# Kernel optimization log

Measured on AMD Instinct MI355X. Metric: run time of the kernel, lower is better.

The kernel has to match this reference:

```python
import jax, jax.numpy as jnp
import numpy as np

N_NODES = 10000
N_EDGES = 160000
K = 3  # Chebyshev filter order
DIMS = [(782, 16), (16, 32), (32, 64), (64, 128), (128, 19)]


def _cheb_norm(edge_index, num_nodes):
    # PyG ChebConv norm with normalization='sym', lambda_max=2.0:
    # scaled Laplacian L_hat = 2L/lambda_max - I = -D^{-1/2} A D^{-1/2} (off-diag), diag = 0
    src, dst = edge_index[0], edge_index[1]
    w = jnp.ones(src.shape, dtype=jnp.float32)
    deg = jax.ops.segment_sum(w, src, num_segments=num_nodes)
    dinv = jnp.where(deg > 0, 1.0 / jnp.sqrt(deg), 0.0)  # masked_fill(inf) -> 0
    return -dinv[src] * dinv[dst]


def _spmm(norm, src, dst, x, num_nodes):
    # out[i] = sum_{e: dst[e]==i} norm[e] * x[src[e]]
    return jax.ops.segment_sum(norm[:, None] * x[src], dst, num_segments=num_nodes)


def _cheb_conv(x, src, dst, norm, W, b):
    # W: [K, Fin, Fout]; Chebyshev recursion T0=x, T1=L_hat x, Tk=2 L_hat T_{k-1} - T_{k-2}
    n = x.shape[0]
    Tx0 = x
    out = Tx0 @ W[0]
    Tx1 = _spmm(norm, src, dst, Tx0, n)
    out = out + Tx1 @ W[1]
    for k in range(2, W.shape[0]):
        Tx2 = 2.0 * _spmm(norm, src, dst, Tx1, n) - Tx0
        out = out + Tx2 @ W[k]
        Tx0, Tx1 = Tx1, Tx2
    return out + b


def setup_inputs() -> dict:
    key = jax.random.key(0)
    ks = jax.random.split(key, 2 + len(DIMS))
    x = jax.random.normal(ks[0], (N_NODES, 782), dtype=jnp.float32)
    edge_index = jax.random.randint(ks[1], (2, N_EDGES), 0, N_NODES)
    inp = {"x": x, "edge_index": edge_index}
    for i, (fi, fo) in enumerate(DIMS):
        inp[f"W{i+1}"] = jax.random.normal(ks[2 + i], (K, fi, fo), dtype=jnp.float32) / np.float32(np.sqrt(fi * K))
        inp[f"b{i+1}"] = jnp.zeros((fo,), dtype=jnp.float32)
    return inp


def reference(x, edge_index, W1, b1, W2, b2, W3, b3, W4, b4, W5, b5):
    src, dst = edge_index[0], edge_index[1]
    norm = _cheb_norm(edge_index, x.shape[0])
    h = jax.nn.relu(_cheb_conv(x, src, dst, norm, W1, b1))
    h = jax.nn.relu(_cheb_conv(h, src, dst, norm, W2, b2))
    h = jax.nn.relu(_cheb_conv(h, src, dst, norm, W3, b3))
    h = jax.nn.relu(_cheb_conv(h, src, dst, norm, W4, b4))
    h = _cheb_conv(h, src, dst, norm, W5, b5)
    return jax.nn.softmax(h, axis=-1)
```

## Files before the change

kernel.cpp:

```cpp
#include <hip/hip_runtime.h>
#include <math.h>

#define NN 10000
#define NE 160000
#define CAP 128
#define NT 256
#define WC1_TOTAL (782 * 48)
#define WC5_TOTAL (128 * 60)
#define L1_SPLITS 12
#define L1_KCHUNK 66
#define CNT_BLKS 625

struct MegaParams {
  const float* x;
  const int* src;
  const int* dst;
  const float* W1; const float* b1;
  const float* W2; const float* b2;
  const float* W3; const float* b3;
  const float* W4; const float* b4;
  const float* W5; const float* b5;
  int* deg; int* cnt; int* bsrc;
  float* dinv; float* wc1; float* wc5;
  float* ABC1; float* E1; float* B2; float* B3; float* B4;
  float* H4; float* ABC5; float* E5; float* P;
  float* out;
};

__device__ __forceinline__ void wcat_one(const float* __restrict__ W,
                                         float* __restrict__ Wc,
                                         int i, int Fin, int F, int Fp) {
  int w3 = 3 * Fp;
  int row = i / w3;
  int c = i - row * w3;
  int sec = c / Fp;
  int f = c - sec * Fp;
  float v = 0.0f;
  if (f < F) {
    if (sec == 0)      v = W[row * F + f] - W[2 * Fin * F + row * F + f];
    else if (sec == 1) v = W[Fin * F + row * F + f];
    else               v = W[2 * Fin * F + row * F + f];
  }
  Wc[i] = v;
}

struct Row8 { float4 lo, hi; };

template <bool AL16>
__device__ __forceinline__ Row8 ld_row8(const float* __restrict__ X, int ldx,
                                        int gr, int M, int kc, int kend) {
  Row8 r;
  r.lo = make_float4(0.f, 0.f, 0.f, 0.f);
  r.hi = make_float4(0.f, 0.f, 0.f, 0.f);
  if (gr < M && kc < kend) {
    const float* xp = X + (size_t)gr * ldx + kc;
    if (kc + 8 <= kend) {
      if (AL16) {
        r.lo = ((const float4*)xp)[0];
        r.hi = ((const float4*)xp)[1];
      } else {
        float2 a = *(const float2*)xp;
        float2 b = *(const float2*)(xp + 2);
        float2 c = *(const float2*)(xp + 4);
        float2 d = *(const float2*)(xp + 6);
        r.lo = make_float4(a.x, a.y, b.x, b.y);
        r.hi = make_float4(c.x, c.y, d.x, d.y);
      }
    } else {
      int rem = kend - kc;
      r.lo.x = xp[0];
      if (rem > 1) r.lo.y = xp[1];
      if (rem > 2) r.lo.z = xp[2];
      if (rem > 3) r.lo.w = xp[3];
      if (rem > 4) r.hi.x = xp[4];
      if (rem > 5) r.hi.y = xp[5];
      if (rem > 6) r.hi.z = xp[6];
    }
  }
  return r;
}

__device__ __forceinline__ float comp8(const Row8& r, int k) {
  switch (k) {
    case 0: return r.lo.x; case 1: return r.lo.y;
    case 2: return r.lo.z; case 3: return r.lo.w;
    case 4: return r.hi.x; case 5: return r.hi.y;
    case 6: return r.hi.z; default: return r.hi.w;
  }
}

__device__ __forceinline__ float rlane(float v, int i) {
  return __int_as_float(__builtin_amdgcn_readlane(__float_as_int(v), i));
}

template <int TN, bool AL16, bool DIRECT>
__device__ void gemm_stage(const float* __restrict__ X, int ldx,
                           const float* __restrict__ W, int ldw,
                           float* __restrict__ Y, int ldy,
                           const float* __restrict__ bias, int relu,
                           int M, int Kd, int Nd, int kchunk, int nk,
                           int tile0, int tstride, float* Ws) {
  int ntR = (M + NT - 1) / NT;
  int ntC = Nd / TN;
  int ntRC = ntR * ntC;
  int ntiles = ntRC * nk;
  constexpr int W4 = TN / 4;
  for (int tile = tile0; tile < ntiles; tile += tstride) {
    int tz = tile / ntRC;
    int rm = tile - tz * ntRC;
    int tc = rm / ntR;
    int tr = rm - tc * ntR;
    int row0 = tr * NT;
    int col0 = tc * TN;
    int k0 = tz * kchunk;
    int kend = k0 + kchunk;
    if (kend > Kd) kend = Kd;
    int k8 = ((kend - k0) + 7) & ~7;
    __syncthreads();
    for (int idx = threadIdx.x; idx < k8 * W4; idx += NT) {
      int wk = idx / W4;
      int wc = (idx - wk * W4) * 4;
      float4 wv = make_float4(0.f, 0.f, 0.f, 0.f);
      if (k0 + wk < kend)
        wv = *(const float4*)(W + (size_t)(k0 + wk) * ldw + col0 + wc);
      *(float4*)(Ws + wk * TN + wc) = wv;
    }
    __syncthreads();
    float acc[TN];
#pragma unroll
    for (int c = 0; c < TN; c++) acc[c] = 0.f;
    int r = row0 + threadIdx.x;
    int nch = k8 >> 3;
    Row8 cur = ld_row8<AL16>(X, ldx, r, M, k0, kend);
    for (int ci = 0; ci < nch; ci++) {
      Row8 nxt = cur;
      if (ci + 1 < nch) nxt = ld_row8<AL16>(X, ldx, r, M, k0 + (ci + 1) * 8, kend);
      int kb = ci << 3;
#pragma unroll
      for (int k = 0; k < 8; k++) {
        float x0 = comp8(cur, k);
        const float* wr = Ws + (kb + k) * TN;
#pragma unroll
        for (int c = 0; c < TN; c += 4) {
          float4 wv = *(const float4*)(wr + c);
          acc[c + 0] += x0 * wv.x; acc[c + 1] += x0 * wv.y;
          acc[c + 2] += x0 * wv.z; acc[c + 3] += x0 * wv.w;
        }
      }
      cur = nxt;
    }
    if (r < M) {
      if (DIRECT) {
        float* yr = Y + (size_t)r * ldy + col0;
#pragma unroll
        for (int c = 0; c < TN; c += 4) {
          float4 v;
          v.x = acc[c + 0] + (bias ? bias[col0 + c + 0] : 0.f);
          v.y = acc[c + 1] + (bias ? bias[col0 + c + 1] : 0.f);
          v.z = acc[c + 2] + (bias ? bias[col0 + c + 2] : 0.f);
          v.w = acc[c + 3] + (bias ? bias[col0 + c + 3] : 0.f);
          if (relu) {
            v.x = fmaxf(v.x, 0.f); v.y = fmaxf(v.y, 0.f);
            v.z = fmaxf(v.z, 0.f); v.w = fmaxf(v.w, 0.f);
          }
          *(float4*)(yr + c) = v;
        }
      } else {
        float* pr = Y + ((size_t)tz * M + r) * Nd + col0;
#pragma unroll
        for (int c = 0; c < TN; c += 4)
          *(float4*)(pr + c) = make_float4(acc[c], acc[c + 1], acc[c + 2], acc[c + 3]);
      }
    }
  }
}

__device__ void spmm_stage(const int* __restrict__ cnt,
                           const int* __restrict__ bsrc,
                           const float* __restrict__ dinv,
                           const float* __restrict__ X, int ldx,
                           float* __restrict__ Y, int ldy,
                           const float* __restrict__ add, int lda,
                           const float* __restrict__ bias,
                           float alpha, float beta,
                           int C_log2, int Fstore, int relu, int do_softmax) {
  int wv = threadIdx.x >> 6;
  int lane = threadIdx.x & 63;
  int C = 1 << C_log2;
  int chunk = lane & (C - 1);
  int eslot = lane >> C_log2;
  int Epar = 64 >> C_log2;
  for (int node = blockIdx.x * 4 + wv; node < NN; node += gridDim.x * 4) {
    int cn = cnt[node]; if (cn > CAP) cn = CAP;
    float dn = dinv[node];
    int j0 = node << 7;
    int j1 = j0 + cn;
    float sx = 0.f, sy = 0.f, sz = 0.f, sw = 0.f;
    for (int j = j0 + eslot; j < j1; j += Epar) {
      int sn = bsrc[j];
      float w = dinv[sn];
      float4 xv = *(const float4*)(X + (size_t)sn * ldx + (chunk << 2));
      sx += w * xv.x; sy += w * xv.y; sz += w * xv.z; sw += w * xv.w;
    }
    for (int st = C; st < 64; st <<= 1) {
      sx += __shfl_xor(sx, st);
      sy += __shfl_xor(sy, st);
      sz += __shfl_xor(sz, st);
      sw += __shfl_xor(sw, st);
    }
    if (eslot == 0) {
      float am = -alpha * dn;
      int f0 = chunk << 2;
      float4 u = make_float4(am * sx, am * sy, am * sz, am * sw);
      if (add) {
        float4 av = *(const float4*)(add + (size_t)node * lda + f0);
        u.x += beta * av.x; u.y += beta * av.y; u.z += beta * av.z; u.w += beta * av.w;
      }
      if (bias) {
        if (f0 + 0 < Fstore) u.x += bias[f0 + 0];
        if (f0 + 1 < Fstore) u.y += bias[f0 + 1];
        if (f0 + 2 < Fstore) u.z += bias[f0 + 2];
        if (f0 + 3 < Fstore) u.w += bias[f0 + 3];
      }
      if (!do_softmax) {
        if (relu) {
          u.x = fmaxf(u.x, 0.f); u.y = fmaxf(u.y, 0.f);
          u.z = fmaxf(u.z, 0.f); u.w = fmaxf(u.w, 0.f);
        }
        if (f0 + 4 <= Fstore) {
          *(float4*)(Y + (size_t)node * ldy + f0) = u;
        } else {
          float vv[4] = {u.x, u.y, u.z, u.w};
#pragma unroll
          for (int c = 0; c < 4; c++)
            if (f0 + c < Fstore) Y[(size_t)node * ldy + f0 + c] = vv[c];
        }
      } else {
        float v[4] = {u.x, u.y, u.z, u.w};
        float mx = -INFINITY;
#pragma unroll
        for (int c = 0; c < 4; c++)
          if (f0 + c < Fstore) mx = fmaxf(mx, v[c]);
        mx = fmaxf(mx, __shfl_xor(mx, 1));
        mx = fmaxf(mx, __shfl_xor(mx, 2));
        mx = fmaxf(mx, __shfl_xor(mx, 4));
        float e[4];
        float s = 0.f;
#pragma unroll
        for (int c = 0; c < 4; c++) {
          e[c] = (f0 + c < Fstore) ? __expf(v[c] - mx) : 0.f;
          s += e[c];
        }
        s += __shfl_xor(s, 1);
        s += __shfl_xor(s, 2);
        s += __shfl_xor(s, 4);
        float inv = 1.f / s;
#pragma unroll
        for (int c = 0; c < 4; c++) {
          int f = f0 + c;
          if (f < Fstore) Y[(size_t)node * ldy + f] = e[c] * inv;
        }
      }
    }
  }
}

template <int F, int C_log2, int LD, int KK, int FOUT, int LDO>
__global__ __launch_bounds__(NT) void k_fused_t2gemm(
    const int* __restrict__ cnt, const int* __restrict__ bsrc,
    const float* __restrict__ dinv, const float* __restrict__ B,
    const float* __restrict__ W, const float* __restrict__ bias,
    float* __restrict__ Y) {
  int wv = threadIdx.x >> 6;
  int lane = threadIdx.x & 63;
  constexpr int C = 1 << C_log2;
  int chunk = lane & (C - 1);
  int eslot = lane >> C_log2;
  constexpr int Epar = 64 >> C_log2;
  int col = lane % FOUT;
  float wr[KK];
#pragma unroll
  for (int k = 0; k < KK; k++) wr[k] = W[k * FOUT + col];
  float bb = bias[col];
  for (int node = blockIdx.x * 4 + wv; node < NN; node += gridDim.x * 4) {
    int cn = cnt[node]; if (cn > CAP) cn = CAP;
    float dn = dinv[node];
    int j0 = node << 7, j1 = j0 + cn;
    float sx = 0.f, sy = 0.f, sz = 0.f, sw = 0.f;
    for (int j = j0 + eslot; j < j1; j += Epar) {
      int sn = bsrc[j];
      float w = dinv[sn];
      float4 xv = *(const float4*)(B + (size_t)sn * LD + F + (chunk << 2));
      sx += w * xv.x; sy += w * xv.y; sz += w * xv.z; sw += w * xv.w;
    }
#pragma unroll
    for (int st = C; st < 64; st <<= 1) {
      sx += __shfl_xor(sx, st);
      sy += __shfl_xor(sy, st);
      sz += __shfl_xor(sz, st);
      sw += __shfl_xor(sw, st);
    }
    int ridx = (lane < 2 * F) ? lane : (lane - 2 * F);
    float rv0 = B[(size_t)node * LD + ridx];
    int f = (KK == 48) ? (lane - 2 * F) : lane;
    int cc = (f >> 2) & (C - 1);
    float a0 = __shfl(sx, cc), a1 = __shfl(sy, cc);
    float a2 = __shfl(sz, cc), a3 = __shfl(sw, cc);
    int comp = f & 3;
    float Ssel = (comp == 0) ? a0 : (comp == 1) ? a1 : (comp == 2) ? a2 : a3;
    float t2v = fmaf(-2.f * dn, Ssel, -rv0);
    float acc = bb;
    if (KK == 48) {
      float rv = (lane < 2 * F) ? rv0 : t2v;
#pragma unroll
      for (int k = 0; k < 48; k++) acc = fmaf(rlane(rv, k), wr[k], acc);
    } else {
#pragma unroll
      for (int k = 0; k < 64; k++) acc = fmaf(rlane(rv0, k), wr[k], acc);
#pragma unroll
      for (int k = 64; k < 96; k++) acc = fmaf(rlane(t2v, k - 64), wr[k], acc);
    }
    acc = fmaxf(acc, 0.f);
    if (lane < FOUT) Y[(size_t)node * LDO + col] = acc;
  }
}

__global__ __launch_bounds__(NT) void k_fused_t2gemm4(
    const int* __restrict__ cnt, const int* __restrict__ bsrc,
    const float* __restrict__ dinv, const float* __restrict__ B,
    const float* __restrict__ W, const float* __restrict__ bias,
    float* __restrict__ Y) {
  __shared__ float t2s[64];
  __shared__ float pacc[128];
  int t = threadIdx.x;
  int wid = t >> 6;
  int lane = t & 63;
  int col = t & 127;
  int kh = t >> 7;
  int chunk = lane & 3;
  int eslot = lane >> 2;
  float wr[96];
#pragma unroll
  for (int k = 0; k < 96; k++) wr[k] = W[(96 * kh + k) * 128 + col];
  float bb = bias[col];
  int foff = 64 + wid * 16 + (chunk << 2);
  for (int node = blockIdx.x; node < NN; node += gridDim.x) {
    int cn = cnt[node]; if (cn > CAP) cn = CAP;
    float dn = dinv[node];
    int j0 = node << 7, j1 = j0 + cn;
    float sx = 0.f, sy = 0.f, sz = 0.f, sw = 0.f;
    for (int j = j0 + eslot; j < j1; j += 16) {
      int sn = bsrc[j];
      float w = dinv[sn];
      float4 xv = *(const float4*)(B + (size_t)sn * 192 + foff);
      sx += w * xv.x; sy += w * xv.y; sz += w * xv.z; sw += w * xv.w;
    }
#pragma unroll
    for (int st = 4; st < 64; st <<= 1) {
      sx += __shfl_xor(sx, st);
      sy += __shfl_xor(sy, st);
      sz += __shfl_xor(sz, st);
      sw += __shfl_xor(sw, st);
    }
    if (eslot == 0) {
      float m = -2.f * dn;
      int o = wid * 16 + (chunk << 2);
      t2s[o + 0] = m * sx;
      t2s[o + 1] = m * sy;
      t2s[o + 2] = m * sz;
      t2s[o + 3] = m * sw;
    }
    float hA = B[(size_t)node * 192 + lane];
    float hB = B[(size_t)node * 192 + 64 + lane];
    __syncthreads();
    float acc = 0.f;
    if (kh == 0) {
#pragma unroll
      for (int k = 0; k < 64; k++) acc = fmaf(rlane(hA, k), wr[k], acc);
#pragma unroll
      for (int k = 64; k < 96; k++) acc = fmaf(rlane(hB, k - 64), wr[k], acc);
    } else {
      float t2v = t2s[lane] - hA;
#pragma unroll
      for (int k = 0; k < 32; k++) acc = fmaf(rlane(hB, 32 + k), wr[k], acc);
#pragma unroll
      for (int k = 32; k < 96; k++) acc = fmaf(rlane(t2v, k - 32), wr[k], acc);
      pacc[col] = acc;
    }
    __syncthreads();
    if (kh == 0) {
      float tot = acc + pacc[col] + bb;
      tot = fmaxf(tot, 0.f);
      Y[(size_t)node * 128 + col] = tot;
    }
    __syncthreads();
  }
}


__global__ __launch_bounds__(NT) void k_zero_wcat(MegaParams p) {
  int tid = blockIdx.x * NT + threadIdx.x;
  int TT = gridDim.x * NT;
  for (int i = tid; i < 2 * NN; i += TT) p.deg[i] = 0;
  for (int i = tid; i < WC1_TOTAL; i += TT) wcat_one(p.W1, p.wc1, i, 782, 16, 16);
  for (int i = tid; i < WC5_TOTAL; i += TT) wcat_one(p.W5, p.wc5, i, 128, 19, 20);
}

__global__ __launch_bounds__(NT) void k_count_gemm1(MegaParams p) {
  __shared__ float Ws[72 * 48];
  if (blockIdx.x < CNT_BLKS) {
    int e = blockIdx.x * NT + threadIdx.x;
    int s = p.src[e], d = p.dst[e];
    atomicAdd(&p.deg[s], 1);
    int slot = atomicAdd(&p.cnt[d], 1);
    if (slot < CAP) p.bsrc[(d << 7) + slot] = s;
  } else {
    gemm_stage<48, false, false>(p.x, 782, p.wc1, 48, p.P, 0, nullptr, 0,
                                 NN, 782, 48, L1_KCHUNK, L1_SPLITS,
                                 blockIdx.x - CNT_BLKS, 1 << 30, Ws);
  }
}

__global__ __launch_bounds__(NT) void k_reduce_dinv(MegaParams p) {
  int tid = blockIdx.x * NT + threadIdx.x;
  int TT = gridDim.x * NT;
  for (int i = tid; i < NN; i += TT) {
    int d = p.deg[i];
    p.dinv[i] = d > 0 ? 1.0f / sqrtf((float)d) : 0.0f;
  }
  for (int i = tid; i < NN * 48; i += TT) {
    float s = 0.f;
#pragma unroll
    for (int z = 0; z < L1_SPLITS; z++) s += p.P[(size_t)z * (NN * 48) + i];
    p.ABC1[i] = s;
  }
}

__global__ __launch_bounds__(NT) void k_spmm(
    const int* cnt, const int* bsrc, const float* dinv,
    const float* X, int ldx, float* Y, int ldy,
    const float* add, int lda, const float* bias,
    float alpha, float beta, int C_log2, int Fstore, int relu, int do_softmax) {
  spmm_stage(cnt, bsrc, dinv, X, ldx, Y, ldy, add, lda, bias,
             alpha, beta, C_log2, Fstore, relu, do_softmax);
}

__global__ __launch_bounds__(NT, 2) void k_gemm20(
    const float* X, int ldx, const float* W, int ldw, float* Y, int ldy,
    const float* bias, int relu, int Kd, int Nd) {
  __shared__ float Ws[128 * 20];
  gemm_stage<20, true, true>(X, ldx, W, ldw, Y, ldy, bias, relu,
                             NN, Kd, Nd, Kd, 1, blockIdx.x, gridDim.x, Ws);
}


extern "C" void kernel_launch(void* const* d_in, const int* in_sizes, int n_in,
                              void* d_out, int out_size, void* d_ws, size_t ws_size,
                              hipStream_t stream) {
  (void)in_sizes; (void)n_in; (void)out_size; (void)ws_size;
  char* p = (char*)d_ws;
  auto alloc = [&](size_t bytes) {
    char* r = p;
    p += (bytes + 255) & ~(size_t)255;
    return r;
  };
  int*   i_deg  = (int*)alloc(sizeof(int) * NN * 2);
  int*   i_bsrc = (int*)alloc(sizeof(int) * NN * CAP);
  float* f_dinv = (float*)alloc(sizeof(float) * NN);
  float* wc1    = (float*)alloc(sizeof(float) * WC1_TOTAL);
  float* wc5    = (float*)alloc(sizeof(float) * WC5_TOTAL);
  float* R1     = (float*)alloc(sizeof(float) * NN * 96);
  float* R2     = (float*)alloc(sizeof(float) * NN * 192);
  float* R3     = (float*)alloc(sizeof(float) * NN * 128);
  float* P      = (float*)alloc(sizeof(float) * NN * 48 * L1_SPLITS);

  MegaParams mp;
  mp.x   = (const float*)d_in[0];
  const int* ei = (const int*)d_in[1];
  mp.src = ei;
  mp.dst = ei + NE;
  mp.W1 = (const float*)d_in[2];  mp.b1 = (const float*)d_in[3];
  mp.W2 = (const float*)d_in[4];  mp.b2 = (const float*)d_in[5];
  mp.W3 = (const float*)d_in[6];  mp.b3 = (const float*)d_in[7];
  mp.W4 = (const float*)d_in[8];  mp.b4 = (const float*)d_in[9];
  mp.W5 = (const float*)d_in[10]; mp.b5 = (const float*)d_in[11];
  mp.deg = i_deg; mp.cnt = i_deg + NN; mp.bsrc = i_bsrc;
  mp.dinv = f_dinv; mp.wc1 = wc1; mp.wc5 = wc5;
  mp.ABC1 = R1; mp.B3 = R1; mp.ABC5 = R1;
  mp.E1 = R2;   mp.B4 = R2; mp.E5 = R2;
  mp.B2 = R3;   mp.H4 = R3;
  mp.P = P;
  mp.out = (float*)d_out;

  k_zero_wcat<<<160, NT, 0, stream>>>(mp);
  k_count_gemm1<<<CNT_BLKS + 480, NT, 0, stream>>>(mp);
  k_reduce_dinv<<<(NN * 48 + NT - 1) / NT, NT, 0, stream>>>(mp);
  k_spmm<<<2500, NT, 0, stream>>>(mp.cnt, mp.bsrc, mp.dinv, mp.ABC1 + 32, 48,
                                  mp.E1, 16, mp.ABC1 + 16, 48, nullptr,
                                  2.f, 1.f, 2, 16, 0, 0);
  k_spmm<<<2500, NT, 0, stream>>>(mp.cnt, mp.bsrc, mp.dinv, mp.E1, 16,
                                  mp.B2, 48, mp.ABC1, 48, mp.b1,
                                  1.f, 1.f, 2, 16, 1, 0);
  k_spmm<<<2500, NT, 0, stream>>>(mp.cnt, mp.bsrc, mp.dinv, mp.B2, 48,
                                  mp.B2 + 16, 48, nullptr, 0, nullptr,
                                  1.f, 0.f, 2, 16, 0, 0);
  k_fused_t2gemm<16, 2, 48, 48, 32, 96><<<1250, NT, 0, stream>>>(
      mp.cnt, mp.bsrc, mp.dinv, mp.B2, mp.W2, mp.b2, mp.B3);
  k_spmm<<<2500, NT, 0, stream>>>(mp.cnt, mp.bsrc, mp.dinv, mp.B3, 96,
                                  mp.B3 + 32, 96, nullptr, 0, nullptr,
                                  1.f, 0.f, 3, 32, 0, 0);
  k_fused_t2gemm<32, 3, 96, 96, 64, 192><<<1250, NT, 0, stream>>>(
      mp.cnt, mp.bsrc, mp.dinv, mp.B3, mp.W3, mp.b3, mp.B4);
  k_spmm<<<2500, NT, 0, stream>>>(mp.cnt, mp.bsrc, mp.dinv, mp.B4, 192,
                                  mp.B4 + 64, 192, nullptr, 0, nullptr,
                                  1.f, 0.f, 4, 64, 0, 0);
  k_fused_t2gemm4<<<2500, NT, 0, stream>>>(
      mp.cnt, mp.bsrc, mp.dinv, mp.B4, mp.W4, mp.b4, mp.H4);
  k_gemm20<<<120, NT, 0, stream>>>(mp.H4, 128, mp.wc5, 60, mp.ABC5, 60, nullptr, 0,
                                   128, 60);
  k_spmm<<<2500, NT, 0, stream>>>(mp.cnt, mp.bsrc, mp.dinv, mp.ABC5 + 40, 60,
                                  mp.E5, 32, mp.ABC5 + 20, 60, nullptr,
                                  2.f, 1.f, 3, 20, 0, 0);
  k_spmm<<<2500, NT, 0, stream>>>(mp.cnt, mp.bsrc, mp.dinv, mp.E5, 32,
                                  mp.out, 19, mp.ABC5, 60, mp.b5,
                                  1.f, 1.f, 3, 19, 0, 1);
}
```

Measured before the change: 269.3 us.

## Replace layer-1 GEMM with coalesced LDS-staged X tiles and readlane-broadcast weights

Replaces the generic gemm_stage for the first-layer x·Wcat product with a dedicated kernel. Each block stages a 64-row by 32-column slice of X into shared memory with coalesced float2 loads. Weights are held in registers and broadcast across the wavefront via readlane, so each lane computes 12 output columns for one row. The K split drops from 12 to 6 chunks with 157 row tiles each, which shrinks the partial-sum buffer that the reduction kernel reads but changes grid size and per-block work.

```diff
diff --git a/kernel.cpp b/kernel.cpp
--- a/kernel.cpp
+++ b/kernel.cpp
@@ -7,8 +7,10 @@
 #define NT 256
 #define WC1_TOTAL (782 * 48)
 #define WC5_TOTAL (128 * 60)
-#define L1_SPLITS 12
-#define L1_KCHUNK 66
+#define L1_SPLITS 6
+#define L1_KCHUNK 132
+#define L1_NTR 157
+#define L1_TILES (L1_NTR * L1_SPLITS)
 #define CNT_BLKS 625
 
 struct MegaParams {
@@ -89,8 +91,82 @@
   }
 }
 
+__device__ __forceinline__ float comp4(const float4& v, int k) {
+  switch (k) {
+    case 0: return v.x; case 1: return v.y; case 2: return v.z; default: return v.w;
+  }
+}
+
 __device__ __forceinline__ float rlane(float v, int i) {
   return __int_as_float(__builtin_amdgcn_readlane(__float_as_int(v), i));
+}
+
+__device__ __forceinline__ float2 ldw8(const float* __restrict__ Wf, int kb,
+                                       int col0, int lc, int lk) {
+  float2 w = make_float2(0.f, 0.f);
+  if (lc < 12) {
+    int k1 = kb + lk, k2 = kb + 4 + lk;
+    if (k1 < 782) w.x = Wf[k1 * 48 + col0 + lc];
+    if (k2 < 782) w.y = Wf[k2 * 48 + col0 + lc];
+  }
+  return w;
+}
+
+__device__ void gemm1_coal(const float* __restrict__ Xg,
+                           const float* __restrict__ Wf,
+                           float* __restrict__ P,
+                           int tile, float (*xs)[36]) {
+  int tz = tile / L1_NTR;
+  int tr = tile - tz * L1_NTR;
+  int row0 = tr * 64;
+  int k0 = tz * L1_KCHUNK;
+  int kend = k0 + L1_KCHUNK;
+  if (kend > 782) kend = 782;
+  int wid = threadIdx.x >> 6, lane = threadIdx.x & 63;
+  int col0 = wid * 12;
+  int lc = lane & 15, lk = lane >> 4;
+  int row = row0 + lane;
+  float acc[12];
+#pragma unroll
+  for (int c = 0; c < 12; c++) acc[c] = 0.f;
+  for (int kc = k0; kc < kend; kc += 32) {
+    __syncthreads();
+    for (int i = threadIdx.x; i < 1024; i += NT) {
+      int r = i >> 4;
+      int c2 = i & 15;
+      int ca = kc + 2 * c2;
+      float2 v = make_float2(0.f, 0.f);
+      if (row0 + r < NN && ca < kend)
+        v = *(const float2*)(Xg + (size_t)(row0 + r) * 782 + ca);
+      *(float2*)&xs[r][2 * c2] = v;
+    }
+    float2 w0 = ldw8(Wf, kc, col0, lc, lk);
+    float2 w1 = ldw8(Wf, kc + 8, col0, lc, lk);
+    float2 w2 = ldw8(Wf, kc + 16, col0, lc, lk);
+    float2 w3 = ldw8(Wf, kc + 24, col0, lc, lk);
+    __syncthreads();
+    float4 xv[8];
+#pragma unroll
+    for (int q = 0; q < 8; q++) xv[q] = *(const float4*)&xs[lane][4 * q];
+#pragma unroll
+    for (int j = 0; j < 4; j++) {
+      float2 ww = (j == 0) ? w0 : (j == 1) ? w1 : (j == 2) ? w2 : w3;
+#pragma unroll
+      for (int kin = 0; kin < 8; kin++) {
+        float x = comp4(xv[j * 2 + (kin >> 2)], kin & 3);
+        float wsrc = (kin < 4) ? ww.x : ww.y;
+#pragma unroll
+        for (int c = 0; c < 12; c++)
+          acc[c] = fmaf(x, rlane(wsrc, (kin & 3) * 16 + c), acc[c]);
+      }
+    }
+  }
+  if (row < NN) {
+    float* pr = P + ((size_t)tz * NN + row) * 48 + col0;
+    *(float4*)(pr + 0) = make_float4(acc[0], acc[1], acc[2], acc[3]);
+    *(float4*)(pr + 4) = make_float4(acc[4], acc[5], acc[6], acc[7]);
+    *(float4*)(pr + 8) = make_float4(acc[8], acc[9], acc[10], acc[11]);
+  }
 }
 
 template <int TN, bool AL16, bool DIRECT>
@@ -407,7 +483,7 @@
 }
 
 __global__ __launch_bounds__(NT) void k_count_gemm1(MegaParams p) {
-  __shared__ float Ws[72 * 48];
+  __shared__ float xs[64][36];
   if (blockIdx.x < CNT_BLKS) {
     int e = blockIdx.x * NT + threadIdx.x;
     int s = p.src[e], d = p.dst[e];
@@ -415,9 +491,7 @@
     int slot = atomicAdd(&p.cnt[d], 1);
     if (slot < CAP) p.bsrc[(d << 7) + slot] = s;
   } else {
-    gemm_stage<48, false, false>(p.x, 782, p.wc1, 48, p.P, 0, nullptr, 0,
-                                 NN, 782, 48, L1_KCHUNK, L1_SPLITS,
-                                 blockIdx.x - CNT_BLKS, 1 << 30, Ws);
+    gemm1_coal(p.x, p.wc1, p.P, blockIdx.x - CNT_BLKS, xs);
   }
 }
 
@@ -493,7 +567,7 @@
   mp.out = (float*)d_out;
 
   k_zero_wcat<<<160, NT, 0, stream>>>(mp);
-  k_count_gemm1<<<CNT_BLKS + 480, NT, 0, stream>>>(mp);
+  k_count_gemm1<<<CNT_BLKS + L1_TILES, NT, 0, stream>>>(mp);
   k_reduce_dinv<<<(NN * 48 + NT - 1) / NT, NT, 0, stream>>>(mp);
   k_spmm<<<2500, NT, 0, stream>>>(mp.cnt, mp.bsrc, mp.dinv, mp.ABC1 + 32, 48,
                                   mp.E1, 16, mp.ABC1 + 16, 48, nullptr,
```

Result: slower. 276.8 us (+2.8%).
